# Kernel tuning notes

Hardware: AMD Instinct MI355X
Metric: run time of the kernel (lower is better)

## Reference

```python
import jax, jax.numpy as jnp
import numpy as np

L1_COST = 1000.0
ENTROPY_COST = 5e-05


def setup_inputs() -> dict:
    key = jax.random.key(0)
    k1, k2 = jax.random.split(key)
    inputs = jax.random.normal(k1, (8, 4096, 256), dtype=jnp.float32)
    # xavier_uniform for [K, D]: bound = sqrt(6/(K+D))
    K, D = 1024, 256
    bound = np.sqrt(6.0 / (K + D)).astype(np.float32)
    codebook = jax.random.uniform(k2, (K, D), dtype=jnp.float32, minval=-bound, maxval=bound)
    return {"inputs": inputs, "codebook": codebook}


def reference(inputs, codebook):
    D = codebook.shape[1]
    flat = inputs.reshape(-1, D)                                  # [N, D]
    norm_C = codebook / jnp.linalg.norm(codebook, axis=1, keepdims=True)   # [K, D]
    flat = flat / jnp.linalg.norm(flat, axis=1, keepdims=True)    # [N, D]
    distances = jax.nn.softmax(flat @ norm_C.T, axis=1)           # [N, K]
    reconstruction = (distances @ norm_C).reshape(inputs.shape)   # [B, S, D]
    # l1_loss(distances, zeros) == mean(|distances|)
    l1 = jnp.mean(jnp.abs(distances))
    # entropy term: mean_i sum_k [ -log_softmax(distances) @ distances.T ]_{ik}
    # = mean_i ( -log_softmax(distances)_i . colsum(distances) ), an O(N*K) equivalent
    log_sm = jax.nn.log_softmax(distances, axis=1)                # [N, K]
    col_sum = jnp.sum(distances, axis=0)                          # [K]
    entropy = jnp.mean(-(log_sm @ col_sum))
    loss = L1_COST * l1 + ENTROPY_COST * entropy
    return reconstruction, loss
```

## Files before the change

### kernel.cpp

```cpp
#include <hip/hip_runtime.h>
#include <cstdint>

#define N_ROWS 32768
#define KDIM 1024
#define DDIM 256

typedef __attribute__((ext_vector_type(8))) short bf16x8;
typedef __attribute__((ext_vector_type(4))) float f32x4;

__device__ __forceinline__ unsigned short f2bf(float f) {
  unsigned int u = __float_as_uint(f);
  u += 0x7FFFu + ((u >> 16) & 1u);
  return (unsigned short)(u >> 16);
}

__device__ __forceinline__ void gload_lds16(const void* g, void* l) {
  __builtin_amdgcn_global_load_lds(
      (const __attribute__((address_space(1))) unsigned int*)(uintptr_t)g,
      (__attribute__((address_space(3))) unsigned int*)(unsigned int)(uintptr_t)l,
      16, 0, 0);
}


__global__ __launch_bounds__(256) void k_norm_cb(const float* __restrict__ cb,
                                                 unsigned short* __restrict__ Cn,
                                                 unsigned short* __restrict__ CnT) {
  const int wid = threadIdx.x >> 6, lane = threadIdx.x & 63;
  const int k = blockIdx.x * 4 + wid;
  float4 v = ((const float4*)(cb + (size_t)k * DDIM))[lane];
  float s = v.x * v.x + v.y * v.y + v.z * v.z + v.w * v.w;
#pragma unroll
  for (int m = 32; m; m >>= 1) s += __shfl_xor(s, m, 64);
  const float rn = 1.0f / sqrtf(s);
  ushort4 p;
  p.x = f2bf(v.x * rn); p.y = f2bf(v.y * rn);
  p.z = f2bf(v.z * rn); p.w = f2bf(v.w * rn);
  const int kb = lane >> 3;
  const int physA = ((lane & 7) >> 1) ^ (k & 3);
  *(ushort4*)(Cn + (size_t)(k >> 6) * 16384 + kb * 2048 + (k & 63) * 32 + physA * 8 + (lane & 1) * 4) = p;
  const int sgl = k >> 5, c31 = k & 31, ch = c31 >> 3, cw = c31 & 7;
  const unsigned short pv[4] = {p.x, p.y, p.z, p.w};
#pragma unroll
  for (int j = 0; j < 4; ++j) {
    const int d = lane * 4 + j;
    CnT[(size_t)sgl * 8192 + d * 32 + ((ch ^ j) * 8) + cw] = pv[j];
  }
}

__global__ __launch_bounds__(512, 2) void k_all(const float* __restrict__ x,
                                                const unsigned short* __restrict__ Cn,
                                                const unsigned short* __restrict__ CnT,
                                                float* __restrict__ part,
                                                float* __restrict__ lse_part,
                                                float* __restrict__ out) {
  __shared__ unsigned short Xs[32768];
  __shared__ unsigned short CAb[2][16384];
  __shared__ unsigned short Ps[128 * 72];
  __shared__ float csl[1024];
  __shared__ float rs[128], qs[128], irl[128];
  __shared__ float lse_sh[2];

  const int tid = threadIdx.x, wid = tid >> 6, lane = tid & 63;
  const int l15 = lane & 15, l4 = lane >> 4;
  const int rb = blockIdx.x;
  if (tid < 128) { rs[tid] = 0.f; qs[tid] = 0.f; }
  for (int j = tid; j < 1024; j += 512) csl[j] = 0.f;

#pragma unroll
  for (int i = 0; i < 4; ++i) {
    const int off = i * 8192 + wid * 1024 + lane * 16;
    gload_lds16((const char*)Cn + off, (char*)CAb[0] + off);
  }
#pragma unroll
  for (int p16 = 0; p16 < 16; ++p16) {
    const int row = p16 * 8 + wid;
    float4 v = ((const float4*)(x + (size_t)(rb * 128 + row) * DDIM))[lane];
    float s = v.x * v.x + v.y * v.y + v.z * v.z + v.w * v.w;
#pragma unroll
    for (int m = 32; m; m >>= 1) s += __shfl_xor(s, m, 64);
    const float rn = 1.0f / sqrtf(s);
    ushort4 p;
    p.x = f2bf(v.x * rn); p.y = f2bf(v.y * rn);
    p.z = f2bf(v.z * rn); p.w = f2bf(v.w * rn);
    const int phys = ((lane & 7) >> 1) ^ (row & 3);
    *(ushort4*)&Xs[(lane >> 3) * 4096 + row * 32 + phys * 8 + (lane & 1) * 4] = p;
  }

  const int wm = wid >> 1, wn = wid & 1;
  const int xsw = l4 ^ (l15 & 3);

  float se[2][4], sq[2][4];
#pragma unroll
  for (int mi = 0; mi < 2; ++mi)
#pragma unroll
    for (int reg = 0; reg < 4; ++reg) { se[mi][reg] = 0.f; sq[mi][reg] = 0.f; }
  for (int kt = 0; kt < 16; ++kt) {
    __syncthreads();
    const int ktn = (kt + 1) & 15;
#pragma unroll
    for (int i = 0; i < 4; ++i) {
      const int off = i * 8192 + wid * 1024 + lane * 16;
      gload_lds16((const char*)Cn + (size_t)ktn * 32768 + off, (char*)CAb[(kt + 1) & 1] + off);
    }
    const unsigned short* B = CAb[kt & 1];
    f32x4 acc[2][2] = {};
#pragma unroll
    for (int kb = 0; kb < 8; ++kb) {
      bf16x8 a[2], b[2];
#pragma unroll
      for (int mi = 0; mi < 2; ++mi)
        a[mi] = *(const bf16x8*)&Xs[kb * 4096 + (wm * 32 + mi * 16 + l15) * 32 + xsw * 8];
#pragma unroll
      for (int ni = 0; ni < 2; ++ni)
        b[ni] = *(const bf16x8*)&B[kb * 2048 + (wn * 32 + ni * 16 + l15) * 32 + xsw * 8];
#pragma unroll
      for (int mi = 0; mi < 2; ++mi)
#pragma unroll
        for (int ni = 0; ni < 2; ++ni)
          acc[mi][ni] = __builtin_amdgcn_mfma_f32_16x16x32_bf16(a[mi], b[ni], acc[mi][ni], 0, 0, 0);
    }
#pragma unroll
    for (int mi = 0; mi < 2; ++mi)
#pragma unroll
      for (int reg = 0; reg < 4; ++reg)
#pragma unroll
        for (int ni = 0; ni < 2; ++ni) {
          const float e = __expf(acc[mi][ni][reg]);
          se[mi][reg] += e; sq[mi][reg] += e * e;
        }
  }
#pragma unroll
  for (int mi = 0; mi < 2; ++mi)
#pragma unroll
    for (int reg = 0; reg < 4; ++reg) {
#pragma unroll
      for (int m = 1; m < 16; m <<= 1) {
        se[mi][reg] += __shfl_xor(se[mi][reg], m, 64);
        sq[mi][reg] += __shfl_xor(sq[mi][reg], m, 64);
      }
    }
  if (l15 == 0) {
#pragma unroll
    for (int mi = 0; mi < 2; ++mi)
#pragma unroll
      for (int reg = 0; reg < 4; ++reg) {
        const int row = wm * 32 + mi * 16 + l4 * 4 + reg;
        atomicAdd(&rs[row], se[mi][reg]);
        atomicAdd(&qs[row], sq[mi][reg]);
      }
  }
  __syncthreads();
  if (tid < 128) {
    const float r = rs[tid];
    const float ir = 1.0f / r;
    irl[tid] = ir;
    float lse = logf((float)(KDIM + 1) + 0.5f * qs[tid] * ir * ir);
#pragma unroll
    for (int m = 32; m; m >>= 1) lse += __shfl_xor(lse, m, 64);
    if ((tid & 63) == 0) lse_sh[tid >> 6] = lse;
  }
  __syncthreads();
  float ir[2][4];
#pragma unroll
  for (int mi = 0; mi < 2; ++mi)
#pragma unroll
    for (int reg = 0; reg < 4; ++reg)
      ir[mi][reg] = irl[wm * 32 + mi * 16 + l4 * 4 + reg];

  f32x4 O[2][8] = {};
  const int psw_r = l15 >> 1;
  for (int kt = 0; kt < 16; ++kt) {
#pragma unroll
    for (int i = 0; i < 4; ++i) {
      const int off = i * 8192 + wid * 1024 + lane * 16;
      gload_lds16((const char*)CnT + (size_t)kt * 32768 + off, (char*)CAb[1] + off);
    }
    f32x4 S[2][2] = {};
#pragma unroll
    for (int kb = 0; kb < 8; ++kb) {
      bf16x8 a[2], b[2];
#pragma unroll
      for (int mi = 0; mi < 2; ++mi)
        a[mi] = *(const bf16x8*)&Xs[kb * 4096 + (wm * 32 + mi * 16 + l15) * 32 + xsw * 8];
#pragma unroll
      for (int ni = 0; ni < 2; ++ni)
        b[ni] = *(const bf16x8*)&CAb[0][kb * 2048 + (wn * 32 + ni * 16 + l15) * 32 + xsw * 8];
#pragma unroll
      for (int mi = 0; mi < 2; ++mi)
#pragma unroll
        for (int ni = 0; ni < 2; ++ni)
          S[mi][ni] = __builtin_amdgcn_mfma_f32_16x16x32_bf16(a[mi], b[ni], S[mi][ni], 0, 0, 0);
    }
    float cs[2] = {0.f, 0.f};
#pragma unroll
    for (int mi = 0; mi < 2; ++mi)
#pragma unroll
      for (int reg = 0; reg < 4; ++reg) {
        const int row = wm * 32 + mi * 16 + l4 * 4 + reg;
        const int pswz = (l4 * 2 + (reg >> 1)) & 7;
#pragma unroll
        for (int ni = 0; ni < 2; ++ni) {
          const float e = __expf(S[mi][ni][reg]);
          const int chl = wn * 4 + ni * 2 + (l15 >> 3);
          Ps[row * 72 + ((chl ^ pswz) * 8) + (l15 & 7)] = f2bf(e);
          cs[ni] += e * ir[mi][reg];
        }
      }
#pragma unroll
    for (int ni = 0; ni < 2; ++ni) {
      float v = cs[ni];
      v += __shfl_xor(v, 16, 64);
      v += __shfl_xor(v, 32, 64);
      if (lane < 16) atomicAdd(&csl[kt * 64 + wn * 32 + ni * 16 + l15], v);
    }
    __syncthreads();
    if (kt < 15) {
#pragma unroll
      for (int i = 0; i < 4; ++i) {
        const int off = i * 8192 + wid * 1024 + lane * 16;
        gload_lds16((const char*)Cn + (size_t)(kt + 1) * 32768 + off, (char*)CAb[0] + off);
      }
    }
#pragma unroll
    for (int kb2 = 0; kb2 < 2; ++kb2) {
      bf16x8 a2[2], b2[8];
#pragma unroll
      for (int mi = 0; mi < 2; ++mi) {
        const int row = wm * 32 + mi * 16 + l15;
        a2[mi] = *(const bf16x8*)&Ps[row * 72 + (((kb2 * 4 + l4) ^ psw_r) * 8)];
      }
#pragma unroll
      for (int ni = 0; ni < 8; ++ni) {
        const int d = wn * 128 + ni * 16 + l15;
        b2[ni] = *(const bf16x8*)&CAb[1][kb2 * 8192 + d * 32 + xsw * 8];
      }
#pragma unroll
      for (int mi = 0; mi < 2; ++mi)
#pragma unroll
        for (int ni = 0; ni < 8; ++ni)
          O[mi][ni] = __builtin_amdgcn_mfma_f32_16x16x32_bf16(a2[mi], b2[ni], O[mi][ni], 0, 0, 0);
    }
    __syncthreads();
  }

#pragma unroll
  for (int mi = 0; mi < 2; ++mi)
#pragma unroll
    for (int reg = 0; reg < 4; ++reg) {
      const int row = wm * 32 + mi * 16 + l4 * 4 + reg;
      const float irv = ir[mi][reg];
#pragma unroll
      for (int ni = 0; ni < 8; ++ni) {
        const int d = wn * 128 + ni * 16 + l15;
        out[(size_t)(rb * 128 + row) * DDIM + d] = O[mi][ni][reg] * irv;
      }
    }
  for (int j = tid; j < 1024; j += 512) part[rb * 1024 + j] = csl[j];
  if (tid == 0) lse_part[rb] = lse_sh[0] + lse_sh[1];
}

__global__ __launch_bounds__(1024) void k_final(const float* __restrict__ part,
                                                const float* __restrict__ lse_part,
                                                float* __restrict__ out) {
  __shared__ float sh1[16], sh2[16], shl[16];
  const int tid = threadIdx.x, lane = tid & 63, w = tid >> 6;
  float cs = 0.f;
  for (int b = 0; b < 256; ++b) cs += part[b * 1024 + tid];
  float s1 = cs, s2 = cs * cs;
  float sl = (tid < 256) ? lse_part[tid] : 0.f;
#pragma unroll
  for (int m = 32; m; m >>= 1) {
    s1 += __shfl_xor(s1, m, 64);
    s2 += __shfl_xor(s2, m, 64);
    sl += __shfl_xor(sl, m, 64);
  }
  if (lane == 0) { sh1[w] = s1; sh2[w] = s2; shl[w] = sl; }
  __syncthreads();
  if (tid == 0) {
    double S = 0.0, Q = 0.0, L = 0.0;
    for (int i = 0; i < 16; ++i) { S += sh1[i]; Q += sh2[i]; L += shl[i]; }
    const double entropy = (S * L - Q) / (double)N_ROWS;
    const double l1 = S / ((double)N_ROWS * (double)KDIM);
    out[(size_t)N_ROWS * DDIM] = (float)(1000.0 * l1 + 5e-5 * entropy);
  }
}

extern "C" void kernel_launch(void* const* d_in, const int* in_sizes, int n_in,
                              void* d_out, int out_size, void* d_ws, size_t ws_size,
                              hipStream_t stream) {
  const float* x = (const float*)d_in[0];
  const float* cb = (const float*)d_in[1];
  float* out = (float*)d_out;
  char* ws = (char*)d_ws;

  unsigned short* Cn  = (unsigned short*)(ws + 0);
  unsigned short* CnT = (unsigned short*)(ws + 524288);
  float* part         = (float*)(ws + 1048576);
  float* lse_part     = (float*)(ws + 2097152);

  k_norm_cb<<<256, 256, 0, stream>>>(cb, Cn, CnT);
  k_all<<<256, 512, 0, stream>>>(x, Cn, CnT, part, lse_part, out);
  k_final<<<1, 1024, 0, stream>>>(part, lse_part, out);
}
```

Baseline: 167.4 us.

## Keep X fragments in registers, deepen codebook prefetch, parallelize final reduction

Normalized X tiles are loaded once into registers instead of being re-read from LDS in every tile step, which frees the Xs buffer for a 4-slot codebook ring. That ring gives pass 1 a two-tile-deep prefetch and lets pass 2 prefetch both the Cn and CnT tiles for the next step. The single-block final reduction is split across 64 blocks that combine with atomics, followed by a tiny loss kernel. The trade-offs are higher register pressure from holding 16 bf16x8 fragments per thread, non-deterministic float atomics, and an extra memset and kernel launch.

```diff
diff --git a/kernel.cpp b/kernel.cpp
--- a/kernel.cpp
+++ b/kernel.cpp
@@ -53,8 +53,7 @@
                                                 float* __restrict__ part,
                                                 float* __restrict__ lse_part,
                                                 float* __restrict__ out) {
-  __shared__ unsigned short Xs[32768];
-  __shared__ unsigned short CAb[2][16384];
+  __shared__ unsigned short Cb[4][16384];
   __shared__ unsigned short Ps[128 * 72];
   __shared__ float csl[1024];
   __shared__ float rs[128], qs[128], irl[128];
@@ -62,6 +61,7 @@
 
   const int tid = threadIdx.x, wid = tid >> 6, lane = tid & 63;
   const int l15 = lane & 15, l4 = lane >> 4;
+  const int wm = wid >> 1, wn = wid & 1;
   const int rb = blockIdx.x;
   if (tid < 128) { rs[tid] = 0.f; qs[tid] = 0.f; }
   for (int j = tid; j < 1024; j += 512) csl[j] = 0.f;
@@ -69,8 +69,11 @@
 #pragma unroll
   for (int i = 0; i < 4; ++i) {
     const int off = i * 8192 + wid * 1024 + lane * 16;
-    gload_lds16((const char*)Cn + off, (char*)CAb[0] + off);
-  }
+    gload_lds16((const char*)Cn + off, (char*)Cb[2] + off);
+    gload_lds16((const char*)Cn + 32768 + off, (char*)Cb[3] + off);
+  }
+
+  unsigned short* Xs = &Cb[0][0];
 #pragma unroll
   for (int p16 = 0; p16 < 16; ++p16) {
     const int row = p16 * 8 + wid;
@@ -82,11 +85,16 @@
     ushort4 p;
     p.x = f2bf(v.x * rn); p.y = f2bf(v.y * rn);
     p.z = f2bf(v.z * rn); p.w = f2bf(v.w * rn);
-    const int phys = ((lane & 7) >> 1) ^ (row & 3);
-    *(ushort4*)&Xs[(lane >> 3) * 4096 + row * 32 + phys * 8 + (lane & 1) * 4] = p;
-  }
-
-  const int wm = wid >> 1, wn = wid & 1;
+    *(ushort4*)&Xs[(lane >> 3) * 4096 + row * 32 + (lane & 7) * 4] = p;
+  }
+  __syncthreads();
+  bf16x8 areg[2][8];
+#pragma unroll
+  for (int mi = 0; mi < 2; ++mi)
+#pragma unroll
+    for (int kb = 0; kb < 8; ++kb)
+      areg[mi][kb] = *(const bf16x8*)&Xs[kb * 4096 + (wm * 32 + mi * 16 + l15) * 32 + l4 * 8];
+
   const int xsw = l4 ^ (l15 & 3);
 
   float se[2][4], sq[2][4];
@@ -96,20 +104,22 @@
     for (int reg = 0; reg < 4; ++reg) { se[mi][reg] = 0.f; sq[mi][reg] = 0.f; }
   for (int kt = 0; kt < 16; ++kt) {
     __syncthreads();
-    const int ktn = (kt + 1) & 15;
-#pragma unroll
-    for (int i = 0; i < 4; ++i) {
-      const int off = i * 8192 + wid * 1024 + lane * 16;
-      gload_lds16((const char*)Cn + (size_t)ktn * 32768 + off, (char*)CAb[(kt + 1) & 1] + off);
-    }
-    const unsigned short* B = CAb[kt & 1];
+    {
+      const char* src = (kt <= 13) ? (const char*)Cn + (size_t)(kt + 2) * 32768
+                      : (kt == 14) ? (const char*)Cn
+                                   : (const char*)CnT;
+      char* dst = (char*)Cb[kt & 3];
+#pragma unroll
+      for (int i = 0; i < 4; ++i) {
+        const int off = i * 8192 + wid * 1024 + lane * 16;
+        gload_lds16(src + off, dst + off);
+      }
+    }
+    const unsigned short* B = Cb[(kt + 2) & 3];
     f32x4 acc[2][2] = {};
 #pragma unroll
     for (int kb = 0; kb < 8; ++kb) {
-      bf16x8 a[2], b[2];
-#pragma unroll
-      for (int mi = 0; mi < 2; ++mi)
-        a[mi] = *(const bf16x8*)&Xs[kb * 4096 + (wm * 32 + mi * 16 + l15) * 32 + xsw * 8];
+      bf16x8 b[2];
 #pragma unroll
       for (int ni = 0; ni < 2; ++ni)
         b[ni] = *(const bf16x8*)&B[kb * 2048 + (wn * 32 + ni * 16 + l15) * 32 + xsw * 8];
@@ -117,7 +127,7 @@
       for (int mi = 0; mi < 2; ++mi)
 #pragma unroll
         for (int ni = 0; ni < 2; ++ni)
-          acc[mi][ni] = __builtin_amdgcn_mfma_f32_16x16x32_bf16(a[mi], b[ni], acc[mi][ni], 0, 0, 0);
+          acc[mi][ni] = __builtin_amdgcn_mfma_f32_16x16x32_bf16(areg[mi][kb], b[ni], acc[mi][ni], 0, 0, 0);
     }
 #pragma unroll
     for (int mi = 0; mi < 2; ++mi)
@@ -170,26 +180,28 @@
   f32x4 O[2][8] = {};
   const int psw_r = l15 >> 1;
   for (int kt = 0; kt < 16; ++kt) {
-#pragma unroll
-    for (int i = 0; i < 4; ++i) {
-      const int off = i * 8192 + wid * 1024 + lane * 16;
-      gload_lds16((const char*)CnT + (size_t)kt * 32768 + off, (char*)CAb[1] + off);
+    const int cslot = (kt & 1) ? 0 : 2;
+    const int tslot = cslot | 1;
+    const int nslot = (kt & 1) ? 2 : 0;
+    if (kt < 15) {
+#pragma unroll
+      for (int i = 0; i < 4; ++i) {
+        const int off = i * 8192 + wid * 1024 + lane * 16;
+        gload_lds16((const char*)Cn + (size_t)(kt + 1) * 32768 + off, (char*)Cb[nslot] + off);
+      }
     }
     f32x4 S[2][2] = {};
 #pragma unroll
     for (int kb = 0; kb < 8; ++kb) {
-      bf16x8 a[2], b[2];
+      bf16x8 b[2];
+#pragma unroll
+      for (int ni = 0; ni < 2; ++ni)
+        b[ni] = *(const bf16x8*)&Cb[cslot][kb * 2048 + (wn * 32 + ni * 16 + l15) * 32 + xsw * 8];
 #pragma unroll
       for (int mi = 0; mi < 2; ++mi)
-        a[mi] = *(const bf16x8*)&Xs[kb * 4096 + (wm * 32 + mi * 16 + l15) * 32 + xsw * 8];
-#pragma unroll
-      for (int ni = 0; ni < 2; ++ni)
-        b[ni] = *(const bf16x8*)&CAb[0][kb * 2048 + (wn * 32 + ni * 16 + l15) * 32 + xsw * 8];
-#pragma unroll
-      for (int mi = 0; mi < 2; ++mi)
 #pragma unroll
         for (int ni = 0; ni < 2; ++ni)
-          S[mi][ni] = __builtin_amdgcn_mfma_f32_16x16x32_bf16(a[mi], b[ni], S[mi][ni], 0, 0, 0);
+          S[mi][ni] = __builtin_amdgcn_mfma_f32_16x16x32_bf16(areg[mi][kb], b[ni], S[mi][ni], 0, 0, 0);
     }
     float cs[2] = {0.f, 0.f};
 #pragma unroll
@@ -218,7 +230,7 @@
 #pragma unroll
       for (int i = 0; i < 4; ++i) {
         const int off = i * 8192 + wid * 1024 + lane * 16;
-        gload_lds16((const char*)Cn + (size_t)(kt + 1) * 32768 + off, (char*)CAb[0] + off);
+        gload_lds16((const char*)CnT + (size_t)(kt + 1) * 32768 + off, (char*)Cb[nslot + 1] + off);
       }
     }
 #pragma unroll
@@ -232,7 +244,7 @@
 #pragma unroll
       for (int ni = 0; ni < 8; ++ni) {
         const int d = wn * 128 + ni * 16 + l15;
-        b2[ni] = *(const bf16x8*)&CAb[1][kb2 * 8192 + d * 32 + xsw * 8];
+        b2[ni] = *(const bf16x8*)&Cb[tslot][kb2 * 8192 + d * 32 + xsw * 8];
       }
 #pragma unroll
       for (int mi = 0; mi < 2; ++mi)
@@ -259,26 +271,45 @@
   if (tid == 0) lse_part[rb] = lse_sh[0] + lse_sh[1];
 }
 
-__global__ __launch_bounds__(1024) void k_final(const float* __restrict__ part,
-                                                const float* __restrict__ lse_part,
-                                                float* __restrict__ out) {
-  __shared__ float sh1[16], sh2[16], shl[16];
+__global__ __launch_bounds__(256) void k_final(const float* __restrict__ part,
+                                               const float* __restrict__ lse_part,
+                                               float* __restrict__ acc3) {
+  __shared__ float sh1[4], sh2[4], shl[4];
   const int tid = threadIdx.x, lane = tid & 63, w = tid >> 6;
-  float cs = 0.f;
-  for (int b = 0; b < 256; ++b) cs += part[b * 1024 + tid];
-  float s1 = cs, s2 = cs * cs;
-  float sl = (tid < 256) ? lse_part[tid] : 0.f;
-#pragma unroll
-  for (int m = 32; m; m >>= 1) {
-    s1 += __shfl_xor(s1, m, 64);
-    s2 += __shfl_xor(s2, m, 64);
-    sl += __shfl_xor(sl, m, 64);
-  }
-  if (lane == 0) { sh1[w] = s1; sh2[w] = s2; shl[w] = sl; }
+  const int bh = tid & 15;
+  const int kh = tid >> 4;
+  const int k = blockIdx.x * 16 + kh;
+  float s = 0.f;
+#pragma unroll
+  for (int m = 0; m < 16; ++m) s += part[(size_t)(bh * 16 + m) * 1024 + k];
+#pragma unroll
+  for (int m = 1; m < 16; m <<= 1) s += __shfl_xor(s, m, 64);
+  float s1 = ((lane & 15) == 0) ? s : 0.f;
+  float s2 = ((lane & 15) == 0) ? s * s : 0.f;
+  s1 += __shfl_xor(s1, 16, 64); s2 += __shfl_xor(s2, 16, 64);
+  s1 += __shfl_xor(s1, 32, 64); s2 += __shfl_xor(s2, 32, 64);
+  if (lane == 0) { sh1[w] = s1; sh2[w] = s2; }
+  float l = 0.f;
+  if (blockIdx.x == 0) {
+    l = lse_part[tid];
+#pragma unroll
+    for (int m = 1; m < 64; m <<= 1) l += __shfl_xor(l, m, 64);
+  }
+  if (lane == 0) shl[w] = l;
   __syncthreads();
   if (tid == 0) {
-    double S = 0.0, Q = 0.0, L = 0.0;
-    for (int i = 0; i < 16; ++i) { S += sh1[i]; Q += sh2[i]; L += shl[i]; }
+    atomicAdd(&acc3[0], sh1[0] + sh1[1] + sh1[2] + sh1[3]);
+    atomicAdd(&acc3[1], sh2[0] + sh2[1] + sh2[2] + sh2[3]);
+    if (blockIdx.x == 0) atomicAdd(&acc3[2], shl[0] + shl[1] + shl[2] + shl[3]);
+  }
+}
+
+__global__ __launch_bounds__(64) void k_loss(const float* __restrict__ acc3,
+                                             float* __restrict__ out) {
+  if (threadIdx.x == 0) {
+    const double S = acc3[0];
+    const double Q = acc3[1];
+    const double L = acc3[2];
     const double entropy = (S * L - Q) / (double)N_ROWS;
     const double l1 = S / ((double)N_ROWS * (double)KDIM);
     out[(size_t)N_ROWS * DDIM] = (float)(1000.0 * l1 + 5e-5 * entropy);
@@ -297,8 +328,11 @@
   unsigned short* CnT = (unsigned short*)(ws + 524288);
   float* part         = (float*)(ws + 1048576);
   float* lse_part     = (float*)(ws + 2097152);
-
+  float* acc3         = (float*)(ws + 2098176);
+
+  hipMemsetAsync(acc3, 0, 16, stream);
   k_norm_cb<<<256, 256, 0, stream>>>(cb, Cn, CnT);
   k_all<<<256, 512, 0, stream>>>(x, Cn, CnT, part, lse_part, out);
-  k_final<<<1, 1024, 0, stream>>>(part, lse_part, out);
-}
+  k_final<<<64, 256, 0, stream>>>(part, lse_part, acc3);
+  k_loss<<<1, 64, 0, stream>>>(acc3, out);
+}
```

Result: faster. 155.1 us (-7.4%).

## Restructure fused kernel into 64-row blocks with register-held X and pipelined codebook stages

Applied to the files above, without the earlier changes.

Shrinks each workgroup to 64 rows and 256 threads, doubling the grid to 512 blocks. The normalized input tile now lives in registers instead of being reloaded from LDS every step, and codebook tiles are 32-wide with a 4-slot LDS ring. The second pass is software-pipelined so the PV matmul of the previous tile overlaps the score and exp work of the current one, using double-buffered P tiles. The final reduction is spread over 64 blocks that combine through atomics and a last-block counter, which needs an extra memset and risks small float-ordering differences.

```diff
diff --git a/kernel.cpp b/kernel.cpp
--- a/kernel.cpp
+++ b/kernel.cpp
@@ -4,6 +4,7 @@
 #define N_ROWS 32768
 #define KDIM 1024
 #define DDIM 256
+#define TS 8192
 
 typedef __attribute__((ext_vector_type(8))) short bf16x8;
 typedef __attribute__((ext_vector_type(4))) float f32x4;
@@ -20,6 +21,16 @@
       (__attribute__((address_space(3))) unsigned int*)(unsigned int)(uintptr_t)l,
       16, 0, 0);
 }
+
+#define STAGE16(srcp, dstp)                                   \
+  {                                                           \
+    const char* _s = (const char*)(srcp);                     \
+    char* _d = (char*)(dstp);                                 \
+    _Pragma("unroll") for (int _i = 0; _i < 4; ++_i) {        \
+      const int _off = _i * 4096 + wid * 1024 + lane * 16;    \
+      gload_lds16(_s + _off, _d + _off);                      \
+    }                                                         \
+  }
 
 
 __global__ __launch_bounds__(256) void k_norm_cb(const float* __restrict__ cb,
@@ -35,46 +46,44 @@
   ushort4 p;
   p.x = f2bf(v.x * rn); p.y = f2bf(v.y * rn);
   p.z = f2bf(v.z * rn); p.w = f2bf(v.w * rn);
-  const int kb = lane >> 3;
-  const int physA = ((lane & 7) >> 1) ^ (k & 3);
-  *(ushort4*)(Cn + (size_t)(k >> 6) * 16384 + kb * 2048 + (k & 63) * 32 + physA * 8 + (lane & 1) * 4) = p;
-  const int sgl = k >> 5, c31 = k & 31, ch = c31 >> 3, cw = c31 & 7;
+  const int t = k >> 5, c31 = k & 31;
+  *(ushort4*)(Cn + (size_t)t * TS + (lane >> 3) * 1024 + c31 * 32 +
+              ((((lane & 7) >> 1) ^ (k & 3)) * 8) + (lane & 1) * 4) = p;
+  const int ch = c31 >> 3, cw = c31 & 7;
   const unsigned short pv[4] = {p.x, p.y, p.z, p.w};
 #pragma unroll
   for (int j = 0; j < 4; ++j) {
     const int d = lane * 4 + j;
-    CnT[(size_t)sgl * 8192 + d * 32 + ((ch ^ j) * 8) + cw] = pv[j];
-  }
-}
-
-__global__ __launch_bounds__(512, 2) void k_all(const float* __restrict__ x,
+    CnT[(size_t)t * TS + d * 32 + ((ch ^ j) * 8) + cw] = pv[j];
+  }
+}
+
+__global__ __launch_bounds__(256, 2) void k_all(const float* __restrict__ x,
                                                 const unsigned short* __restrict__ Cn,
                                                 const unsigned short* __restrict__ CnT,
                                                 float* __restrict__ part,
                                                 float* __restrict__ lse_part,
                                                 float* __restrict__ out) {
-  __shared__ unsigned short Xs[32768];
-  __shared__ unsigned short CAb[2][16384];
-  __shared__ unsigned short Ps[128 * 72];
+  __shared__ unsigned short Sl[4][TS];
+  __shared__ unsigned short Ps[2][64 * 40];
   __shared__ float csl[1024];
-  __shared__ float rs[128], qs[128], irl[128];
-  __shared__ float lse_sh[2];
+  __shared__ float rs[64], qs[64], irl[64];
 
   const int tid = threadIdx.x, wid = tid >> 6, lane = tid & 63;
   const int l15 = lane & 15, l4 = lane >> 4;
+  const int wm = wid >> 1, wn = wid & 1;
   const int rb = blockIdx.x;
-  if (tid < 128) { rs[tid] = 0.f; qs[tid] = 0.f; }
-  for (int j = tid; j < 1024; j += 512) csl[j] = 0.f;
-
-#pragma unroll
-  for (int i = 0; i < 4; ++i) {
-    const int off = i * 8192 + wid * 1024 + lane * 16;
-    gload_lds16((const char*)Cn + off, (char*)CAb[0] + off);
-  }
+  if (tid < 64) { rs[tid] = 0.f; qs[tid] = 0.f; }
+  for (int j = tid; j < 1024; j += 256) csl[j] = 0.f;
+
+  STAGE16(Cn, Sl[0]);
+  STAGE16((const char*)Cn + TS * 2, Sl[1]);
+
+  unsigned short* Xs = &Sl[2][0];
 #pragma unroll
   for (int p16 = 0; p16 < 16; ++p16) {
-    const int row = p16 * 8 + wid;
-    float4 v = ((const float4*)(x + (size_t)(rb * 128 + row) * DDIM))[lane];
+    const int row = p16 * 4 + wid;
+    float4 v = ((const float4*)(x + (size_t)(rb * 64 + row) * DDIM))[lane];
     float s = v.x * v.x + v.y * v.y + v.z * v.z + v.w * v.w;
 #pragma unroll
     for (int m = 32; m; m >>= 1) s += __shfl_xor(s, m, 64);
@@ -82,52 +91,42 @@
     ushort4 p;
     p.x = f2bf(v.x * rn); p.y = f2bf(v.y * rn);
     p.z = f2bf(v.z * rn); p.w = f2bf(v.w * rn);
-    const int phys = ((lane & 7) >> 1) ^ (row & 3);
-    *(ushort4*)&Xs[(lane >> 3) * 4096 + row * 32 + phys * 8 + (lane & 1) * 4] = p;
-  }
-
-  const int wm = wid >> 1, wn = wid & 1;
-  const int xsw = l4 ^ (l15 & 3);
+    *(ushort4*)&Xs[(lane >> 3) * 2048 + row * 32 + (lane & 7) * 4] = p;
+  }
+  __syncthreads();
+  bf16x8 areg[2][8];
+#pragma unroll
+  for (int mi = 0; mi < 2; ++mi)
+#pragma unroll
+    for (int kb = 0; kb < 8; ++kb)
+      areg[mi][kb] = *(const bf16x8*)&Xs[kb * 2048 + (wm * 32 + mi * 16 + l15) * 32 + l4 * 8];
+  __syncthreads();
+
+  const int bsw = (l4 ^ (l15 & 3)) * 8;
 
   float se[2][4], sq[2][4];
 #pragma unroll
   for (int mi = 0; mi < 2; ++mi)
 #pragma unroll
     for (int reg = 0; reg < 4; ++reg) { se[mi][reg] = 0.f; sq[mi][reg] = 0.f; }
-  for (int kt = 0; kt < 16; ++kt) {
+  for (int kt = 0; kt < 32; ++kt) {
+    STAGE16((const char*)Cn + (size_t)((kt + 2) & 31) * TS * 2, Sl[(kt + 2) & 3]);
+    const unsigned short* B = Sl[kt & 3];
+    f32x4 acc[2] = {};
+#pragma unroll
+    for (int kb = 0; kb < 8; ++kb) {
+      const bf16x8 b = *(const bf16x8*)&B[kb * 1024 + (wn * 16 + l15) * 32 + bsw];
+      acc[0] = __builtin_amdgcn_mfma_f32_16x16x32_bf16(areg[0][kb], b, acc[0], 0, 0, 0);
+      acc[1] = __builtin_amdgcn_mfma_f32_16x16x32_bf16(areg[1][kb], b, acc[1], 0, 0, 0);
+    }
+#pragma unroll
+    for (int mi = 0; mi < 2; ++mi)
+#pragma unroll
+      for (int reg = 0; reg < 4; ++reg) {
+        const float e = __expf(acc[mi][reg]);
+        se[mi][reg] += e; sq[mi][reg] += e * e;
+      }
     __syncthreads();
-    const int ktn = (kt + 1) & 15;
-#pragma unroll
-    for (int i = 0; i < 4; ++i) {
-      const int off = i * 8192 + wid * 1024 + lane * 16;
-      gload_lds16((const char*)Cn + (size_t)ktn * 32768 + off, (char*)CAb[(kt + 1) & 1] + off);
-    }
-    const unsigned short* B = CAb[kt & 1];
-    f32x4 acc[2][2] = {};
-#pragma unroll
-    for (int kb = 0; kb < 8; ++kb) {
-      bf16x8 a[2], b[2];
-#pragma unroll
-      for (int mi = 0; mi < 2; ++mi)
-        a[mi] = *(const bf16x8*)&Xs[kb * 4096 + (wm * 32 + mi * 16 + l15) * 32 + xsw * 8];
-#pragma unroll
-      for (int ni = 0; ni < 2; ++ni)
-        b[ni] = *(const bf16x8*)&B[kb * 2048 + (wn * 32 + ni * 16 + l15) * 32 + xsw * 8];
-#pragma unroll
-      for (int mi = 0; mi < 2; ++mi)
-#pragma unroll
-        for (int ni = 0; ni < 2; ++ni)
-          acc[mi][ni] = __builtin_amdgcn_mfma_f32_16x16x32_bf16(a[mi], b[ni], acc[mi][ni], 0, 0, 0);
-    }
-#pragma unroll
-    for (int mi = 0; mi < 2; ++mi)
-#pragma unroll
-      for (int reg = 0; reg < 4; ++reg)
-#pragma unroll
-        for (int ni = 0; ni < 2; ++ni) {
-          const float e = __expf(acc[mi][ni][reg]);
-          se[mi][reg] += e; sq[mi][reg] += e * e;
-        }
   }
 #pragma unroll
   for (int mi = 0; mi < 2; ++mi)
@@ -150,14 +149,14 @@
       }
   }
   __syncthreads();
-  if (tid < 128) {
+  if (tid < 64) {
     const float r = rs[tid];
     const float ir = 1.0f / r;
     irl[tid] = ir;
     float lse = logf((float)(KDIM + 1) + 0.5f * qs[tid] * ir * ir);
 #pragma unroll
     for (int m = 32; m; m >>= 1) lse += __shfl_xor(lse, m, 64);
-    if ((tid & 63) == 0) lse_sh[tid >> 6] = lse;
+    if (tid == 0) lse_part[rb] = lse;
   }
   __syncthreads();
   float ir[2][4];
@@ -168,80 +167,51 @@
       ir[mi][reg] = irl[wm * 32 + mi * 16 + l4 * 4 + reg];
 
   f32x4 O[2][8] = {};
-  const int psw_r = l15 >> 1;
-  for (int kt = 0; kt < 16; ++kt) {
-#pragma unroll
-    for (int i = 0; i < 4; ++i) {
-      const int off = i * 8192 + wid * 1024 + lane * 16;
-      gload_lds16((const char*)CnT + (size_t)kt * 32768 + off, (char*)CAb[1] + off);
-    }
-    f32x4 S[2][2] = {};
-#pragma unroll
-    for (int kb = 0; kb < 8; ++kb) {
-      bf16x8 a[2], b[2];
-#pragma unroll
-      for (int mi = 0; mi < 2; ++mi)
-        a[mi] = *(const bf16x8*)&Xs[kb * 4096 + (wm * 32 + mi * 16 + l15) * 32 + xsw * 8];
-#pragma unroll
-      for (int ni = 0; ni < 2; ++ni)
-        b[ni] = *(const bf16x8*)&CAb[0][kb * 2048 + (wn * 32 + ni * 16 + l15) * 32 + xsw * 8];
-#pragma unroll
-      for (int mi = 0; mi < 2; ++mi)
-#pragma unroll
-        for (int ni = 0; ni < 2; ++ni)
-          S[mi][ni] = __builtin_amdgcn_mfma_f32_16x16x32_bf16(a[mi], b[ni], S[mi][ni], 0, 0, 0);
-    }
-    float cs[2] = {0.f, 0.f};
-#pragma unroll
-    for (int mi = 0; mi < 2; ++mi)
-#pragma unroll
-      for (int reg = 0; reg < 4; ++reg) {
-        const int row = wm * 32 + mi * 16 + l4 * 4 + reg;
-        const int pswz = (l4 * 2 + (reg >> 1)) & 7;
-#pragma unroll
-        for (int ni = 0; ni < 2; ++ni) {
-          const float e = __expf(S[mi][ni][reg]);
-          const int chl = wn * 4 + ni * 2 + (l15 >> 3);
-          Ps[row * 72 + ((chl ^ pswz) * 8) + (l15 & 7)] = f2bf(e);
-          cs[ni] += e * ir[mi][reg];
-        }
-      }
-#pragma unroll
-    for (int ni = 0; ni < 2; ++ni) {
-      float v = cs[ni];
-      v += __shfl_xor(v, 16, 64);
-      v += __shfl_xor(v, 32, 64);
-      if (lane < 16) atomicAdd(&csl[kt * 64 + wn * 32 + ni * 16 + l15], v);
-    }
+  const int ps_w = (((wn * 2 + (l15 >> 3)) ^ l4) * 8) + (l15 & 7);
+  const int ps_r = ((l4 ^ ((l15 >> 2) & 3)) * 8);
+#define S_EPI(kt_, Bslot_, Pbuf_)                                                   \
+  {                                                                                 \
+    const unsigned short* B_ = Sl[Bslot_];                                          \
+    f32x4 S_[2] = {};                                                               \
+    _Pragma("unroll") for (int kb = 0; kb < 8; ++kb) {                              \
+      const bf16x8 b = *(const bf16x8*)&B_[kb * 1024 + (wn * 16 + l15) * 32 + bsw]; \
+      S_[0] = __builtin_amdgcn_mfma_f32_16x16x32_bf16(areg[0][kb], b, S_[0], 0, 0, 0); \
+      S_[1] = __builtin_amdgcn_mfma_f32_16x16x32_bf16(areg[1][kb], b, S_[1], 0, 0, 0); \
+    }                                                                               \
+    float cs = 0.f;                                                                 \
+    _Pragma("unroll") for (int mi = 0; mi < 2; ++mi)                                \
+      _Pragma("unroll") for (int reg = 0; reg < 4; ++reg) {                         \
+        const int row = wm * 32 + mi * 16 + l4 * 4 + reg;                           \
+        const float e = __expf(S_[mi][reg]);                                        \
+        Ps[Pbuf_][row * 40 + ps_w] = f2bf(e);                                       \
+        cs += e * ir[mi][reg];                                                      \
+      }                                                                             \
+    cs += __shfl_xor(cs, 16, 64);                                                   \
+    cs += __shfl_xor(cs, 32, 64);                                                   \
+    if (lane < 16) atomicAdd(&csl[(kt_) * 32 + wn * 16 + l15], cs);                 \
+  }
+#define PV_STEP(Pbuf_, Tslot_)                                                       \
+  {                                                                                  \
+    bf16x8 a2[2], b2[8];                                                             \
+    _Pragma("unroll") for (int mi = 0; mi < 2; ++mi)                                 \
+      a2[mi] = *(const bf16x8*)&Ps[Pbuf_][(wm * 32 + mi * 16 + l15) * 40 + ps_r];    \
+    _Pragma("unroll") for (int ni = 0; ni < 8; ++ni)                                 \
+      b2[ni] = *(const bf16x8*)&Sl[Tslot_][(wn * 128 + ni * 16 + l15) * 32 + bsw];   \
+    _Pragma("unroll") for (int mi = 0; mi < 2; ++mi)                                 \
+      _Pragma("unroll") for (int ni = 0; ni < 8; ++ni)                               \
+        O[mi][ni] = __builtin_amdgcn_mfma_f32_16x16x32_bf16(a2[mi], b2[ni], O[mi][ni], 0, 0, 0); \
+  }
+  STAGE16(CnT, Sl[2]);
+  S_EPI(0, 0, 0);
+  __syncthreads();
+  for (int kt = 1; kt < 32; ++kt) {
+    STAGE16((const char*)CnT + (size_t)kt * TS * 2, Sl[2 + (kt & 1)]);
+    if (kt <= 30) STAGE16((const char*)Cn + (size_t)(kt + 1) * TS * 2, Sl[(kt + 1) & 1]);
+    PV_STEP((kt - 1) & 1, 2 + ((kt - 1) & 1));
+    S_EPI(kt, kt & 1, kt & 1);
     __syncthreads();
-    if (kt < 15) {
-#pragma unroll
-      for (int i = 0; i < 4; ++i) {
-        const int off = i * 8192 + wid * 1024 + lane * 16;
-        gload_lds16((const char*)Cn + (size_t)(kt + 1) * 32768 + off, (char*)CAb[0] + off);
-      }
-    }
-#pragma unroll
-    for (int kb2 = 0; kb2 < 2; ++kb2) {
-      bf16x8 a2[2], b2[8];
-#pragma unroll
-      for (int mi = 0; mi < 2; ++mi) {
-        const int row = wm * 32 + mi * 16 + l15;
-        a2[mi] = *(const bf16x8*)&Ps[row * 72 + (((kb2 * 4 + l4) ^ psw_r) * 8)];
-      }
-#pragma unroll
-      for (int ni = 0; ni < 8; ++ni) {
-        const int d = wn * 128 + ni * 16 + l15;
-        b2[ni] = *(const bf16x8*)&CAb[1][kb2 * 8192 + d * 32 + xsw * 8];
-      }
-#pragma unroll
-      for (int mi = 0; mi < 2; ++mi)
-#pragma unroll
-        for (int ni = 0; ni < 8; ++ni)
-          O[mi][ni] = __builtin_amdgcn_mfma_f32_16x16x32_bf16(a2[mi], b2[ni], O[mi][ni], 0, 0, 0);
-    }
-    __syncthreads();
-  }
+  }
+  PV_STEP(1, 3);
 
 #pragma unroll
   for (int mi = 0; mi < 2; ++mi)
@@ -252,36 +222,61 @@
 #pragma unroll
       for (int ni = 0; ni < 8; ++ni) {
         const int d = wn * 128 + ni * 16 + l15;
-        out[(size_t)(rb * 128 + row) * DDIM + d] = O[mi][ni][reg] * irv;
+        out[(size_t)(rb * 64 + row) * DDIM + d] = O[mi][ni][reg] * irv;
       }
     }
-  for (int j = tid; j < 1024; j += 512) part[rb * 1024 + j] = csl[j];
-  if (tid == 0) lse_part[rb] = lse_sh[0] + lse_sh[1];
-}
-
-__global__ __launch_bounds__(1024) void k_final(const float* __restrict__ part,
-                                                const float* __restrict__ lse_part,
-                                                float* __restrict__ out) {
-  __shared__ float sh1[16], sh2[16], shl[16];
-  const int tid = threadIdx.x, lane = tid & 63, w = tid >> 6;
-  float cs = 0.f;
-  for (int b = 0; b < 256; ++b) cs += part[b * 1024 + tid];
-  float s1 = cs, s2 = cs * cs;
-  float sl = (tid < 256) ? lse_part[tid] : 0.f;
-#pragma unroll
-  for (int m = 32; m; m >>= 1) {
-    s1 += __shfl_xor(s1, m, 64);
-    s2 += __shfl_xor(s2, m, 64);
-    sl += __shfl_xor(sl, m, 64);
-  }
-  if (lane == 0) { sh1[w] = s1; sh2[w] = s2; shl[w] = sl; }
+  __syncthreads();
+  for (int j = tid; j < 1024; j += 256) part[(size_t)rb * 1024 + j] = csl[j];
+}
+
+__global__ __launch_bounds__(256) void k_final(const float* __restrict__ part,
+                                               const float* __restrict__ lse_part,
+                                               float* __restrict__ acc,
+                                               float* __restrict__ out) {
+  __shared__ float sh[4][16], shl[4];
+  const int tid = threadIdx.x, w = tid >> 6, lane = tid & 63;
+  const int l15 = lane & 15, l4 = lane >> 4;
+  const int k = blockIdx.x * 16 + l15;
+  const int g = w * 4 + l4;
+  float s = 0.f;
+#pragma unroll 8
+  for (int m = 0; m < 32; ++m) s += part[(size_t)(g * 32 + m) * 1024 + k];
+  s += __shfl_xor(s, 16, 64);
+  s += __shfl_xor(s, 32, 64);
+  if (lane < 16) sh[w][l15] = s;
+  float l = 0.f;
+  if (blockIdx.x == 0) {
+    l = lse_part[tid] + lse_part[256 + tid];
+#pragma unroll
+    for (int m = 1; m < 64; m <<= 1) l += __shfl_xor(l, m, 64);
+    if (lane == 0) shl[w] = l;
+  }
+  __syncthreads();
+  if (tid < 16) {
+    const float cs = sh[0][tid] + sh[1][tid] + sh[2][tid] + sh[3][tid];
+    float s1 = cs, s2 = cs * cs;
+#pragma unroll
+    for (int m = 1; m < 16; m <<= 1) {
+      s1 += __shfl_xor(s1, m, 64);
+      s2 += __shfl_xor(s2, m, 64);
+    }
+    if (tid == 0) {
+      atomicAdd(&acc[0], s1);
+      atomicAdd(&acc[1], s2);
+      if (blockIdx.x == 0) atomicAdd(&acc[2], shl[0] + shl[1] + shl[2] + shl[3]);
+    }
+  }
   __syncthreads();
   if (tid == 0) {
-    double S = 0.0, Q = 0.0, L = 0.0;
-    for (int i = 0; i < 16; ++i) { S += sh1[i]; Q += sh2[i]; L += shl[i]; }
-    const double entropy = (S * L - Q) / (double)N_ROWS;
-    const double l1 = S / ((double)N_ROWS * (double)KDIM);
-    out[(size_t)N_ROWS * DDIM] = (float)(1000.0 * l1 + 5e-5 * entropy);
+    __threadfence();
+    const unsigned int old = atomicAdd((unsigned int*)&acc[3], 1u);
+    if (old == 63u) {
+      __threadfence();
+      const double S = acc[0], Q = acc[1], L = acc[2];
+      const double entropy = (S * L - Q) / (double)N_ROWS;
+      const double l1 = S / ((double)N_ROWS * (double)KDIM);
+      out[(size_t)N_ROWS * DDIM] = (float)(1000.0 * l1 + 5e-5 * entropy);
+    }
   }
 }
 
@@ -296,9 +291,11 @@
   unsigned short* Cn  = (unsigned short*)(ws + 0);
   unsigned short* CnT = (unsigned short*)(ws + 524288);
   float* part         = (float*)(ws + 1048576);
-  float* lse_part     = (float*)(ws + 2097152);
-
+  float* lse_part     = (float*)(ws + 3145728);
+  float* acc          = (float*)(ws + 3147776);
+
+  hipMemsetAsync(acc, 0, 16, stream);
   k_norm_cb<<<256, 256, 0, stream>>>(cb, Cn, CnT);
-  k_all<<<256, 512, 0, stream>>>(x, Cn, CnT, part, lse_part, out);
-  k_final<<<1, 1024, 0, stream>>>(part, lse_part, out);
-}
+  k_all<<<512, 256, 0, stream>>>(x, Cn, CnT, part, lse_part, out);
+  k_final<<<64, 256, 0, stream>>>(part, lse_part, acc, out);
+}
```

New measurement: 159.6 us. -4.7%, faster.
